# Kernel tuning notes

Hardware: AMD Instinct MI355X
Metric: run time of the kernel (lower is better)

The kernel has to match this reference:

```python
import jax, jax.numpy as jnp
import numpy as np

EMB = 2048
H = 16
Q_RANK = 1536
KV_RANK = 512
ROPE_D = 64
NOPE_D = 64
V_D = 128
QK_D = ROPE_D + NOPE_D  # 128
ROPE_BASE = 10000.0
SCALING = 1.0  # query_pre_attn_scalar ** -0.5 with scalar=1.0


def apply_rope(x):
    """torchtune-style interleaved RoPE. x: (B, S, H, D)."""
    S, D = x.shape[1], x.shape[-1]
    theta = 1.0 / (ROPE_BASE ** (jnp.arange(0, D, 2, dtype=jnp.float32) / D))  # (D/2,)
    ang = jnp.arange(S, dtype=jnp.float32)[:, None] * theta[None, :]  # (S, D/2)
    cos = jnp.cos(ang)[None, :, None, :]
    sin = jnp.sin(ang)[None, :, None, :]
    xf = x.astype(jnp.float32).reshape(*x.shape[:-1], D // 2, 2)
    x0, x1 = xf[..., 0], xf[..., 1]
    out = jnp.stack([x0 * cos - x1 * sin, x1 * cos + x0 * sin], axis=-1)
    return out.reshape(x.shape).astype(x.dtype)


def setup_inputs() -> dict:
    key = jax.random.key(0)
    ks = jax.random.split(key, 6)
    s = lambda fan_in: 1.0 / np.sqrt(fan_in)
    return {
        "x": jax.random.normal(ks[0], (2, 2048, EMB), dtype=jnp.float32),
        "q_a_w": jax.random.uniform(ks[1], (Q_RANK, EMB), jnp.float32, -s(EMB), s(EMB)),
        "q_b_w": jax.random.uniform(ks[2], (H * QK_D, Q_RANK), jnp.float32, -s(Q_RANK), s(Q_RANK)),
        "kv_a_w": jax.random.uniform(ks[3], (KV_RANK + ROPE_D, EMB), jnp.float32, -s(EMB), s(EMB)),
        "kv_b_w": jax.random.uniform(ks[4], (H * (NOPE_D + V_D), KV_RANK), jnp.float32, -s(KV_RANK), s(KV_RANK)),
        "o_w": jax.random.uniform(ks[5], (EMB, H * V_D), jnp.float32, -s(H * V_D), s(H * V_D)),
    }


def reference(x, q_a_w, q_b_w, kv_a_w, kv_b_w, o_w):
    B, S, _ = x.shape
    # LoRA-compressed Q projection
    q = (x @ q_a_w.T) @ q_b_w.T  # (B, S, H*QK_D)
    q = q.reshape(B, S, H, QK_D).transpose(0, 2, 1, 3)  # (B, H, S, QK_D)
    q_pass, q_rot = q[..., :NOPE_D], q[..., NOPE_D:]
    # Compressed KV with shared rope key
    ckv = x @ kv_a_w.T  # (B, S, KV_RANK + ROPE_D)
    k_pass_c, k_rot = ckv[..., :KV_RANK], ckv[..., KV_RANK:]
    kvb = (k_pass_c @ kv_b_w.T).reshape(B, S, H, NOPE_D + V_D).transpose(0, 2, 1, 3)
    k_pass, v = kvb[..., :NOPE_D], kvb[..., NOPE_D:]  # (B,H,S,NOPE_D), (B,H,S,V_D)
    # RoPE (applied in (B,S,H,D) layout, as in the original)
    q_rot = apply_rope(q_rot.transpose(0, 2, 1, 3)).transpose(0, 2, 1, 3)
    k_rot = apply_rope(k_rot[:, :, None, :])  # (B, S, 1, ROPE_D), shared across heads
    k_rot = jnp.broadcast_to(k_rot.transpose(0, 2, 1, 3), (B, H, S, ROPE_D))
    query = jnp.concatenate([q_pass, q_rot], axis=-1)  # (B, H, S, QK_D)
    key = jnp.concatenate([k_pass, k_rot], axis=-1)
    # NOTE: original passes attention_mask=None -> no causal mask applied.
    scores = jnp.einsum("bhqd,bhkd->bhqk", query, key) * SCALING
    attn = jax.nn.softmax(scores.astype(jnp.float32), axis=-1).astype(query.dtype)
    out = jnp.einsum("bhqk,bhkd->bhqd", attn, v)  # (B, H, S, V_D)
    out = out.transpose(0, 2, 1, 3).reshape(B, S, H * V_D)
    return out @ o_w.T
```

## Files before the change

kernel.cpp:

```cpp
#include <hip/hip_runtime.h>
#include <stdint.h>

#define EMB 2048
#define NH 16
#define QRANK 1536
#define KVRANK 512
#define ROPED 64
#define NOPED 64
#define VD 128
#define QKD 128
#define SEQ 2048
#define BATCH 2
#define BS 4096
#define BHD 32
#define NCOMB 2112

typedef __attribute__((ext_vector_type(4))) float f32x4;
typedef __attribute__((ext_vector_type(8))) short s16x8;

__device__ __forceinline__ float bf2f(unsigned short u) {
  return __uint_as_float(((unsigned int)u) << 16);
}
__device__ __forceinline__ unsigned short f2bf(float f) {
  unsigned int u = __float_as_uint(f);
  u += 0x7fff + ((u >> 16) & 1);
  return (unsigned short)(u >> 16);
}

__device__ __forceinline__ void gld_lds16(const unsigned short* g, unsigned short* l) {
  __builtin_amdgcn_global_load_lds((const __attribute__((address_space(1))) void*)g,
                                   (__attribute__((address_space(3))) void*)l,
                                   16, 0, 0);
}

#define N4_X   (BS * EMB / 4)
#define N4_QA  (QRANK * EMB / 4)
#define N4_KVA ((KVRANK + ROPED) * EMB / 4)
#define N4_QB  (NH * QKD * QRANK / 4)
#define N4_KVB (NH * 192 * KVRANK / 4)
#define N4_O   (EMB * NH * VD / 4)
#define N4_TOT (N4_X + N4_QA + N4_KVA + N4_QB + N4_KVB + N4_O)

__global__ void cast_all(const float* __restrict__ x, const float* __restrict__ qa,
                         const float* __restrict__ kva, const float* __restrict__ qb,
                         const float* __restrict__ kvb, const float* __restrict__ ow,
                         unsigned short* __restrict__ Xb, unsigned short* __restrict__ Wcomb,
                         unsigned short* __restrict__ Wqb, unsigned short* __restrict__ Wkvb,
                         unsigned short* __restrict__ Wo) {
  int i = blockIdx.x * blockDim.x + threadIdx.x;
  int stride = gridDim.x * blockDim.x;
  for (; i < N4_TOT; i += stride) {
    const float4* src;
    ushort4* dst;
    int j = i;
    if (j < N4_X) { src = (const float4*)x; dst = (ushort4*)Xb; }
    else if ((j -= N4_X) < N4_QA) { src = (const float4*)qa; dst = (ushort4*)Wcomb; }
    else if ((j -= N4_QA) < N4_KVA) { src = (const float4*)kva; dst = (ushort4*)(Wcomb + (size_t)QRANK * EMB); }
    else if ((j -= N4_KVA) < N4_QB) { src = (const float4*)qb; dst = (ushort4*)Wqb; }
    else if ((j -= N4_QB) < N4_KVB) { src = (const float4*)kvb; dst = (ushort4*)Wkvb; }
    else { j -= N4_KVB; src = (const float4*)ow; dst = (ushort4*)Wo; }
    float4 v = src[j];
    ushort4 o;
    o.x = f2bf(v.x); o.y = f2bf(v.y); o.z = f2bf(v.z); o.w = f2bf(v.w);
    dst[j] = o;
  }
}

template <int OUT_F32>
__global__ __launch_bounds__(256, 2) void gemm_bt(
    const unsigned short* __restrict__ A, int lda,
    const unsigned short* __restrict__ W, int ldw,
    void* __restrict__ C, int M, int N, int K)
{
  __shared__ __align__(16) unsigned short As[128 * 64];
  __shared__ __align__(16) unsigned short Ws[128 * 64];
  const int tid = threadIdx.x;
  const int wave = tid >> 6;
  const int lane = tid & 63;
  const int ln = lane & 15;
  const int quad = lane >> 4;
  const int bm = blockIdx.y * 128;
  const int bn = blockIdx.x * 128;
  const int wm = (wave >> 1) * 64;
  const int wn = (wave & 1) * 64;

  f32x4 acc[4][4] = {};

  const int rel8 = lane >> 3;
  const int csw = ((lane & 7) ^ rel8) * 8;

  for (int k0 = 0; k0 < K; k0 += 64) {
#pragma unroll
    for (int it = 0; it < 4; ++it) {
      int rb = wave * 32 + it * 8;
      gld_lds16(A + (size_t)(bm + rb + rel8) * lda + k0 + csw, &As[rb * 64]);
    }
#pragma unroll
    for (int it = 0; it < 4; ++it) {
      int rb = wave * 32 + it * 8;
      int wr = bn + rb + rel8;
      if (wr >= N) wr = N - 1;
      gld_lds16(W + (size_t)wr * ldw + k0 + csw, &Ws[rb * 64]);
    }
    __syncthreads();
#pragma unroll
    for (int kk = 0; kk < 64; kk += 32) {
      s16x8 a[4], b[4];
#pragma unroll
      for (int mt = 0; mt < 4; ++mt)
        a[mt] = *(const s16x8*)&As[(wm + mt * 16 + ln) * 64 + ((kk / 8 + quad) ^ (ln & 7)) * 8];
#pragma unroll
      for (int nt = 0; nt < 4; ++nt)
        b[nt] = *(const s16x8*)&Ws[(wn + nt * 16 + ln) * 64 + ((kk / 8 + quad) ^ (ln & 7)) * 8];
#pragma unroll
      for (int mt = 0; mt < 4; ++mt)
#pragma unroll
        for (int nt = 0; nt < 4; ++nt)
          acc[mt][nt] = __builtin_amdgcn_mfma_f32_16x16x32_bf16(a[mt], b[nt], acc[mt][nt], 0, 0, 0);
    }
    __syncthreads();
  }
#pragma unroll
  for (int mt = 0; mt < 4; ++mt) {
    int row = bm + wm + mt * 16 + quad * 4;
#pragma unroll
    for (int nt = 0; nt < 4; ++nt) {
      int col = bn + wn + nt * 16 + ln;
      if (col < N) {
#pragma unroll
        for (int r = 0; r < 4; ++r) {
          float v = acc[mt][nt][r];
          if (OUT_F32)
            ((float*)C)[(size_t)(row + r) * N + col] = v;
          else
            ((unsigned short*)C)[(size_t)(row + r) * N + col] = f2bf(v);
        }
      }
    }
  }
}

__global__ __launch_bounds__(256, 2) void gemm_q_rope(
    const unsigned short* __restrict__ A, int lda,
    const unsigned short* __restrict__ W, int ldw,
    unsigned short* __restrict__ Qry, int K)
{
  __shared__ __align__(16) unsigned short As[128 * 64];
  __shared__ __align__(16) unsigned short Ws[128 * 64];
  const int tid = threadIdx.x;
  const int wave = tid >> 6;
  const int lane = tid & 63;
  const int ln = lane & 15;
  const int quad = lane >> 4;
  const int bm = blockIdx.y * 128;
  const int bn = blockIdx.x * 128;
  const int wm = (wave >> 1) * 64;
  const int wn = (wave & 1) * 64;

  f32x4 acc[4][4] = {};
  const int rel8 = lane >> 3;
  const int csw = ((lane & 7) ^ rel8) * 8;

  for (int k0 = 0; k0 < K; k0 += 64) {
#pragma unroll
    for (int it = 0; it < 4; ++it) {
      int rb = wave * 32 + it * 8;
      gld_lds16(A + (size_t)(bm + rb + rel8) * lda + k0 + csw, &As[rb * 64]);
    }
#pragma unroll
    for (int it = 0; it < 4; ++it) {
      int rb = wave * 32 + it * 8;
      gld_lds16(W + (size_t)(bn + rb + rel8) * ldw + k0 + csw, &Ws[rb * 64]);
    }
    __syncthreads();
#pragma unroll
    for (int kk = 0; kk < 64; kk += 32) {
      s16x8 a[4], b[4];
#pragma unroll
      for (int mt = 0; mt < 4; ++mt)
        a[mt] = *(const s16x8*)&As[(wm + mt * 16 + ln) * 64 + ((kk / 8 + quad) ^ (ln & 7)) * 8];
#pragma unroll
      for (int nt = 0; nt < 4; ++nt)
        b[nt] = *(const s16x8*)&Ws[(wn + nt * 16 + ln) * 64 + ((kk / 8 + quad) ^ (ln & 7)) * 8];
#pragma unroll
      for (int mt = 0; mt < 4; ++mt)
#pragma unroll
        for (int nt = 0; nt < 4; ++nt)
          acc[mt][nt] = __builtin_amdgcn_mfma_f32_16x16x32_bf16(a[mt], b[nt], acc[mt][nt], 0, 0, 0);
    }
    __syncthreads();
  }
  const bool odd = (ln & 1);
#pragma unroll
  for (int mt = 0; mt < 4; ++mt) {
    int rowb = bm + wm + mt * 16 + quad * 4;
#pragma unroll
    for (int nt = 0; nt < 4; ++nt) {
      int col = bn + wn + nt * 16 + ln;
      int h = col >> 7, d = col & 127;
#pragma unroll
      for (int r = 0; r < 4; ++r) {
        float v = acc[mt][nt][r];
        float other = __shfl_xor(v, 1);
        int row = rowb + r;
        int b = row >> 11, s = row & 2047;
        float y = v;
        if (d >= NOPED) {
          int i = (d - NOPED) >> 1;
          float theta = exp2f(-(float)i * (13.287712379549449f / 32.f));
          float ang = (float)s * theta;
          float sn, c;
          sincosf(ang, &sn, &c);
          y = v * c + (odd ? other * sn : -other * sn);
        }
        Qry[((size_t)(b * NH + h) * SEQ + s) * QKD + d] = f2bf(y);
      }
    }
  }
}

__global__ void prep_key(const unsigned short* __restrict__ kvb,
                         const unsigned short* __restrict__ cqkv,
                         unsigned short* __restrict__ Key) {
  __shared__ unsigned short krot[ROPED];
  int bs = blockIdx.x;
  int b = bs >> 11, s = bs & 2047;
  int tid = threadIdx.x;
  if (tid < 32) {
    int i = tid;
    float x0 = bf2f(cqkv[(size_t)bs * NCOMB + QRANK + KVRANK + 2 * i]);
    float x1 = bf2f(cqkv[(size_t)bs * NCOMB + QRANK + KVRANK + 2 * i + 1]);
    float theta = exp2f(-(float)i * (13.287712379549449f / 32.f));
    float ang = (float)s * theta;
    float sn, c;
    sincosf(ang, &sn, &c);
    krot[2 * i] = f2bf(x0 * c - x1 * sn);
    krot[2 * i + 1] = f2bf(x1 * c + x0 * sn);
  }
  __syncthreads();
  for (int idx = tid; idx < NH * QKD; idx += 256) {
    int h = idx >> 7, d = idx & 127;
    unsigned short v;
    if (d < NOPED)
      v = kvb[(size_t)bs * (NH * 192) + h * 192 + d];
    else
      v = krot[d - NOPED];
    Key[((size_t)(b * NH + h) * SEQ + s) * QKD + d] = v;
  }
}

__global__ void transpose_v(const unsigned short* __restrict__ kvb, unsigned short* __restrict__ VT) {
  __shared__ unsigned short tile[64][132];
  int blk = blockIdx.x;
  int bh = blk >> 5, st = blk & 31;
  int b = bh >> 4, h = bh & 15;
  int s0 = st * 64;
  int tid = threadIdx.x;
  for (int idx = tid; idx < 64 * 128; idx += 256) {
    int sl = idx >> 7, d = idx & 127;
    tile[sl][d] = kvb[((size_t)(b * SEQ + s0 + sl)) * (NH * 192) + h * 192 + NOPED + d];
  }
  __syncthreads();
  for (int idx = tid; idx < 64 * 128; idx += 256) {
    int d = idx >> 6, sl = idx & 63;
    VT[((size_t)bh * VD + d) * SEQ + s0 + sl] = tile[sl][d];
  }
}

__global__ __launch_bounds__(256, 2) void flash_attn(
    const unsigned short* __restrict__ Q,
    const unsigned short* __restrict__ Kt,
    const unsigned short* __restrict__ VT,
    unsigned short* __restrict__ O)
{
  __shared__ __align__(16) unsigned short Ks[64 * 128];
  __shared__ __align__(16) unsigned short Vs[128 * 64];
  __shared__ __align__(16) unsigned short Ps[4 * 2048];

  const int tid = threadIdx.x;
  const int wave = tid >> 6;
  const int lane = tid & 63;
  const int ln = lane & 15;
  const int quad = lane >> 4;
  const int bh = blockIdx.x;
  const int q0 = blockIdx.y * 128;

  s16x8 qa[2][4];
#pragma unroll
  for (int mt = 0; mt < 2; ++mt) {
    const unsigned short* qrow = Q + ((size_t)bh * SEQ + q0 + wave * 32 + mt * 16 + ln) * QKD;
#pragma unroll
    for (int kx = 0; kx < 4; ++kx)
      qa[mt][kx] = *(const s16x8*)(qrow + kx * 32 + quad * 8);
  }

  unsigned short* Pw = &Ps[wave * 2048];

  f32x4 o[2][8] = {};
  float m_i[2][4], l_i[2][4];
#pragma unroll
  for (int mt = 0; mt < 2; ++mt)
#pragma unroll
    for (int r = 0; r < 4; ++r) { m_i[mt][r] = -1e30f; l_i[mt][r] = 0.f; }

  const bool even = ((ln & 1) == 0);

  for (int kt = 0; kt < SEQ / 64; ++kt) {
    {
      int rel = lane >> 4, cch = lane & 15;
#pragma unroll
      for (int it = 0; it < 4; ++it) {
        int rb = wave * 16 + it * 4;
        int rr = rb + rel;
        int c = cch ^ (rr & 15);
        gld_lds16(Kt + ((size_t)bh * SEQ + kt * 64 + rr) * QKD + c * 8, &Ks[rb * 128]);
      }
      int rel8 = lane >> 3;
      int c8 = (lane & 7) ^ rel8;
#pragma unroll
      for (int it = 0; it < 4; ++it) {
        int rb = wave * 32 + it * 8;
        gld_lds16(VT + ((size_t)bh * VD + rb + rel8) * SEQ + kt * 64 + c8 * 8, &Vs[rb * 64]);
      }
    }
    __syncthreads();

    f32x4 sc[2][4] = {};
#pragma unroll
    for (int kx = 0; kx < 4; ++kx) {
      s16x8 bk[4];
#pragma unroll
      for (int t = 0; t < 4; ++t)
        bk[t] = *(const s16x8*)&Ks[(t * 16 + ln) * 128 + ((kx * 4 + quad) ^ ln) * 8];
#pragma unroll
      for (int mt = 0; mt < 2; ++mt)
#pragma unroll
        for (int t = 0; t < 4; ++t)
          sc[mt][t] = __builtin_amdgcn_mfma_f32_16x16x32_bf16(qa[mt][kx], bk[t], sc[mt][t], 0, 0, 0);
    }

    float al[2][4];
#pragma unroll
    for (int mt = 0; mt < 2; ++mt) {
      float mx[4], rs[4];
#pragma unroll
      for (int r = 0; r < 4; ++r)
        mx[r] = fmaxf(fmaxf(sc[mt][0][r], sc[mt][1][r]), fmaxf(sc[mt][2][r], sc[mt][3][r]));
#pragma unroll
      for (int msk = 1; msk < 16; msk <<= 1)
#pragma unroll
        for (int r = 0; r < 4; ++r)
          mx[r] = fmaxf(mx[r], __shfl_xor(mx[r], msk));
#pragma unroll
      for (int r = 0; r < 4; ++r) {
        float mn = fmaxf(m_i[mt][r], mx[r]);
        al[mt][r] = __expf(m_i[mt][r] - mn);
        m_i[mt][r] = mn;
        rs[r] = 0.f;
      }
#pragma unroll
      for (int t = 0; t < 4; ++t)
#pragma unroll
        for (int r = 0; r < 4; ++r) {
          float e = __expf(sc[mt][t][r] - m_i[mt][r]);
          sc[mt][t][r] = e;
          rs[r] += e;
        }
#pragma unroll
      for (int msk = 1; msk < 16; msk <<= 1)
#pragma unroll
        for (int r = 0; r < 4; ++r)
          rs[r] += __shfl_xor(rs[r], msk);
#pragma unroll
      for (int r = 0; r < 4; ++r)
        l_i[mt][r] = l_i[mt][r] * al[mt][r] + rs[r];
#pragma unroll
      for (int dt = 0; dt < 8; ++dt)
#pragma unroll
        for (int r = 0; r < 4; ++r)
          o[mt][dt][r] *= al[mt][r];
    }

#pragma unroll
    for (int mt = 0; mt < 2; ++mt)
#pragma unroll
      for (int t = 0; t < 4; ++t) {
        unsigned int pu[4], nu[4];
#pragma unroll
        for (int r = 0; r < 4; ++r) {
          pu[r] = __float_as_uint(sc[mt][t][r]);
          nu[r] = __float_as_uint(__shfl_xor(sc[mt][t][r], 1));
        }
        if (even) {
          int cb = t * 2 + (ln >> 3);
          int rbase = mt * 16 + quad * 4;
#pragma unroll
          for (int rp = 0; rp < 2; ++rp) {
            int swc = cb ^ (quad * 2 + rp);
            unsigned short* a = &Pw[(rbase + 2 * rp) * 64 + swc * 8 + (ln & 7)];
            *(unsigned int*)a        = (pu[2 * rp] >> 16)     | (nu[2 * rp] & 0xffff0000u);
            *(unsigned int*)(a + 64) = (pu[2 * rp + 1] >> 16) | (nu[2 * rp + 1] & 0xffff0000u);
          }
        }
      }
    asm volatile("s_waitcnt lgkmcnt(0)" ::: "memory");

#pragma unroll
    for (int kc = 0; kc < 2; ++kc) {
      s16x8 ap[2];
#pragma unroll
      for (int mt = 0; mt < 2; ++mt)
        ap[mt] = *(const s16x8*)&Pw[(mt * 16 + ln) * 64 + ((kc * 4 + quad) ^ (ln >> 1)) * 8];
#pragma unroll
      for (int dt = 0; dt < 8; ++dt) {
        s16x8 bv = *(const s16x8*)&Vs[(dt * 16 + ln) * 64 + ((kc * 4 + quad) ^ (ln & 7)) * 8];
#pragma unroll
        for (int mt = 0; mt < 2; ++mt)
          o[mt][dt] = __builtin_amdgcn_mfma_f32_16x16x32_bf16(ap[mt], bv, o[mt][dt], 0, 0, 0);
      }
    }
    __syncthreads();
  }

  const int b = bh >> 4, h = bh & 15;
#pragma unroll
  for (int mt = 0; mt < 2; ++mt)
#pragma unroll
    for (int r = 0; r < 4; ++r) {
      float inv = 1.f / l_i[mt][r];
      int s = q0 + wave * 32 + mt * 16 + quad * 4 + r;
      size_t rowbase = ((size_t)b * SEQ + s) * (NH * VD) + h * VD;
#pragma unroll
      for (int dt = 0; dt < 8; ++dt)
        O[rowbase + dt * 16 + ln] = f2bf(o[mt][dt][r] * inv);
    }
}

extern "C" void kernel_launch(void* const* d_in, const int* in_sizes, int n_in,
                              void* d_out, int out_size, void* d_ws, size_t ws_size,
                              hipStream_t stream) {
  const float* x_f    = (const float*)d_in[0];
  const float* qaw_f  = (const float*)d_in[1];
  const float* qbw_f  = (const float*)d_in[2];
  const float* kvaw_f = (const float*)d_in[3];
  const float* kvbw_f = (const float*)d_in[4];
  const float* ow_f   = (const float*)d_in[5];

  char* ws = (char*)d_ws;
  size_t off = 0;
  auto alloc = [&](size_t n) {
    unsigned short* p = (unsigned short*)(ws + off);
    off = (off + n * 2 + 255) & ~(size_t)255;
    return p;
  };
  unsigned short* Xb    = alloc((size_t)BS * EMB);
  unsigned short* Wcomb = alloc((size_t)NCOMB * EMB);
  unsigned short* Wqb   = alloc((size_t)(NH * QKD) * QRANK);
  unsigned short* Wkvb  = alloc((size_t)(NH * 192) * KVRANK);
  unsigned short* Wo    = alloc((size_t)EMB * (NH * VD));
  unsigned short* CQKV  = alloc((size_t)BS * NCOMB);
  unsigned short* KVB   = alloc((size_t)BS * (NH * 192));
  unsigned short* Qry   = alloc((size_t)BHD * SEQ * QKD);
  unsigned short* Key   = alloc((size_t)BHD * SEQ * QKD);
  unsigned short* Vt    = alloc((size_t)BHD * VD * SEQ);
  unsigned short* AO    = alloc((size_t)BS * (NH * VD));

  cast_all<<<dim3(8192), 256, 0, stream>>>(x_f, qaw_f, kvaw_f, qbw_f, kvbw_f, ow_f,
                                           Xb, Wcomb, Wqb, Wkvb, Wo);

  gemm_bt<0><<<dim3((NCOMB + 127) / 128, BS / 128), 256, 0, stream>>>(
      Xb, EMB, Wcomb, EMB, CQKV, BS, NCOMB, EMB);
  gemm_q_rope<<<dim3((NH * QKD) / 128, BS / 128), 256, 0, stream>>>(
      CQKV, NCOMB, Wqb, QRANK, Qry, QRANK);
  gemm_bt<0><<<dim3((NH * 192) / 128, BS / 128), 256, 0, stream>>>(
      CQKV + QRANK, NCOMB, Wkvb, KVRANK, KVB, BS, NH * 192, KVRANK);

  prep_key<<<dim3(BS), 256, 0, stream>>>(KVB, CQKV, Key);
  transpose_v<<<dim3(BHD * (SEQ / 64)), 256, 0, stream>>>(KVB, Vt);

  flash_attn<<<dim3(BHD, SEQ / 128), 256, 0, stream>>>(Qry, Key, Vt, AO);

  gemm_bt<1><<<dim3(EMB / 128, BS / 128), 256, 0, stream>>>(
      AO, NH * VD, Wo, NH * VD, d_out, BS, EMB, NH * VD);
}
```

Baseline: 432.7 us.

## Compute transposed scores to keep P in registers, dropping LDS round-trip

```diff
diff --git a/kernel.cpp b/kernel.cpp
--- a/kernel.cpp
+++ b/kernel.cpp
@@ -17,6 +17,7 @@
 
 typedef __attribute__((ext_vector_type(4))) float f32x4;
 typedef __attribute__((ext_vector_type(8))) short s16x8;
+typedef __attribute__((ext_vector_type(4))) short s16x4;
 
 __device__ __forceinline__ float bf2f(unsigned short u) {
   return __uint_as_float(((unsigned int)u) << 16);
@@ -25,6 +26,14 @@
   unsigned int u = __float_as_uint(f);
   u += 0x7fff + ((u >> 16) & 1);
   return (unsigned short)(u >> 16);
+}
+
+__device__ __forceinline__ f32x4 mfma16k16(s16x4 a, s16x4 b, f32x4 c) {
+#if __has_builtin(__builtin_amdgcn_mfma_f32_16x16x16_bf16)
+  return __builtin_amdgcn_mfma_f32_16x16x16_bf16(a, b, c, 0, 0, 0);
+#else
+  return __builtin_amdgcn_mfma_f32_16x16x16bf16_1k(a, b, c, 0, 0, 0);
+#endif
 }
 
 __device__ __forceinline__ void gld_lds16(const unsigned short* g, unsigned short* l) {
@@ -275,7 +284,6 @@
 {
   __shared__ __align__(16) unsigned short Ks[64 * 128];
   __shared__ __align__(16) unsigned short Vs[128 * 64];
-  __shared__ __align__(16) unsigned short Ps[4 * 2048];
 
   const int tid = threadIdx.x;
   const int wave = tid >> 6;
@@ -294,16 +302,9 @@
       qa[mt][kx] = *(const s16x8*)(qrow + kx * 32 + quad * 8);
   }
 
-  unsigned short* Pw = &Ps[wave * 2048];
-
   f32x4 o[2][8] = {};
-  float m_i[2][4], l_i[2][4];
-#pragma unroll
-  for (int mt = 0; mt < 2; ++mt)
-#pragma unroll
-    for (int r = 0; r < 4; ++r) { m_i[mt][r] = -1e30f; l_i[mt][r] = 0.f; }
-
-  const bool even = ((ln & 1) == 0);
+  float m_i[2] = {-1e30f, -1e30f};
+  float l_i[2] = {0.f, 0.f};
 
   for (int kt = 0; kt < SEQ / 64; ++kt) {
     {
@@ -328,95 +329,63 @@
     f32x4 sc[2][4] = {};
 #pragma unroll
     for (int kx = 0; kx < 4; ++kx) {
-      s16x8 bk[4];
+      s16x8 ak[4];
 #pragma unroll
       for (int t = 0; t < 4; ++t)
-        bk[t] = *(const s16x8*)&Ks[(t * 16 + ln) * 128 + ((kx * 4 + quad) ^ ln) * 8];
+        ak[t] = *(const s16x8*)&Ks[(t * 16 + ln) * 128 + ((kx * 4 + quad) ^ ln) * 8];
 #pragma unroll
       for (int mt = 0; mt < 2; ++mt)
 #pragma unroll
         for (int t = 0; t < 4; ++t)
-          sc[mt][t] = __builtin_amdgcn_mfma_f32_16x16x32_bf16(qa[mt][kx], bk[t], sc[mt][t], 0, 0, 0);
-    }
-
-    float al[2][4];
+          sc[mt][t] = __builtin_amdgcn_mfma_f32_16x16x32_bf16(ak[t], qa[mt][kx], sc[mt][t], 0, 0, 0);
+    }
+
+    s16x4 pb[2][4];
 #pragma unroll
     for (int mt = 0; mt < 2; ++mt) {
-      float mx[4], rs[4];
-#pragma unroll
-      for (int r = 0; r < 4; ++r)
-        mx[r] = fmaxf(fmaxf(sc[mt][0][r], sc[mt][1][r]), fmaxf(sc[mt][2][r], sc[mt][3][r]));
-#pragma unroll
-      for (int msk = 1; msk < 16; msk <<= 1)
+      float mx = sc[mt][0][0];
+#pragma unroll
+      for (int t = 0; t < 4; ++t)
 #pragma unroll
         for (int r = 0; r < 4; ++r)
-          mx[r] = fmaxf(mx[r], __shfl_xor(mx[r], msk));
-#pragma unroll
-      for (int r = 0; r < 4; ++r) {
-        float mn = fmaxf(m_i[mt][r], mx[r]);
-        al[mt][r] = __expf(m_i[mt][r] - mn);
-        m_i[mt][r] = mn;
-        rs[r] = 0.f;
-      }
-#pragma unroll
-      for (int t = 0; t < 4; ++t)
-#pragma unroll
-        for (int r = 0; r < 4; ++r) {
-          float e = __expf(sc[mt][t][r] - m_i[mt][r]);
-          sc[mt][t][r] = e;
-          rs[r] += e;
-        }
-#pragma unroll
-      for (int msk = 1; msk < 16; msk <<= 1)
+          mx = fmaxf(mx, sc[mt][t][r]);
+      mx = fmaxf(mx, __shfl_xor(mx, 16));
+      mx = fmaxf(mx, __shfl_xor(mx, 32));
+      float mn = fmaxf(m_i[mt], mx);
+      float al = __expf(m_i[mt] - mn);
+      m_i[mt] = mn;
+      float rs = 0.f;
+#pragma unroll
+      for (int t = 0; t < 4; ++t) {
+        float e0 = __expf(sc[mt][t][0] - mn);
+        float e1 = __expf(sc[mt][t][1] - mn);
+        float e2 = __expf(sc[mt][t][2] - mn);
+        float e3 = __expf(sc[mt][t][3] - mn);
+        rs += (e0 + e1) + (e2 + e3);
+        s16x4 p;
+        p[0] = (short)f2bf(e0); p[1] = (short)f2bf(e1);
+        p[2] = (short)f2bf(e2); p[3] = (short)f2bf(e3);
+        pb[mt][t] = p;
+      }
+      rs += __shfl_xor(rs, 16);
+      rs += __shfl_xor(rs, 32);
+      l_i[mt] = l_i[mt] * al + rs;
+#pragma unroll
+      for (int dt = 0; dt < 8; ++dt)
 #pragma unroll
         for (int r = 0; r < 4; ++r)
-          rs[r] += __shfl_xor(rs[r], msk);
-#pragma unroll
-      for (int r = 0; r < 4; ++r)
-        l_i[mt][r] = l_i[mt][r] * al[mt][r] + rs[r];
-#pragma unroll
-      for (int dt = 0; dt < 8; ++dt)
-#pragma unroll
-        for (int r = 0; r < 4; ++r)
-          o[mt][dt][r] *= al[mt][r];
-    }
-
-#pragma unroll
-    for (int mt = 0; mt < 2; ++mt)
-#pragma unroll
-      for (int t = 0; t < 4; ++t) {
-        unsigned int pu[4], nu[4];
-#pragma unroll
-        for (int r = 0; r < 4; ++r) {
-          pu[r] = __float_as_uint(sc[mt][t][r]);
-          nu[r] = __float_as_uint(__shfl_xor(sc[mt][t][r], 1));
-        }
-        if (even) {
-          int cb = t * 2 + (ln >> 3);
-          int rbase = mt * 16 + quad * 4;
-#pragma unroll
-          for (int rp = 0; rp < 2; ++rp) {
-            int swc = cb ^ (quad * 2 + rp);
-            unsigned short* a = &Pw[(rbase + 2 * rp) * 64 + swc * 8 + (ln & 7)];
-            *(unsigned int*)a        = (pu[2 * rp] >> 16)     | (nu[2 * rp] & 0xffff0000u);
-            *(unsigned int*)(a + 64) = (pu[2 * rp + 1] >> 16) | (nu[2 * rp + 1] & 0xffff0000u);
-          }
-        }
-      }
-    asm volatile("s_waitcnt lgkmcnt(0)" ::: "memory");
-
-#pragma unroll
-    for (int kc = 0; kc < 2; ++kc) {
-      s16x8 ap[2];
-#pragma unroll
-      for (int mt = 0; mt < 2; ++mt)
-        ap[mt] = *(const s16x8*)&Pw[(mt * 16 + ln) * 64 + ((kc * 4 + quad) ^ (ln >> 1)) * 8];
+          o[mt][dt][r] *= al;
+    }
+
+#pragma unroll
+    for (int kc = 0; kc < 4; ++kc) {
+      int gsl = ((kc * 2 + (quad >> 1)) ^ (ln & 7)) * 8 + (quad & 1) * 4;
 #pragma unroll
       for (int dt = 0; dt < 8; ++dt) {
-        s16x8 bv = *(const s16x8*)&Vs[(dt * 16 + ln) * 64 + ((kc * 4 + quad) ^ (ln & 7)) * 8];
+        s16x4 av = *(const s16x4*)&Vs[(dt * 16 + ln) * 64 + gsl];
 #pragma unroll
         for (int mt = 0; mt < 2; ++mt)
-          o[mt][dt] = __builtin_amdgcn_mfma_f32_16x16x32_bf16(ap[mt], bv, o[mt][dt], 0, 0, 0);
+          o[mt][dt] = mfma16k16(av, pb[mt][kc], o[mt][dt]);
       }
     }
     __syncthreads();
@@ -424,16 +393,20 @@
 
   const int b = bh >> 4, h = bh & 15;
 #pragma unroll
-  for (int mt = 0; mt < 2; ++mt)
-#pragma unroll
-    for (int r = 0; r < 4; ++r) {
-      float inv = 1.f / l_i[mt][r];
-      int s = q0 + wave * 32 + mt * 16 + quad * 4 + r;
-      size_t rowbase = ((size_t)b * SEQ + s) * (NH * VD) + h * VD;
-#pragma unroll
-      for (int dt = 0; dt < 8; ++dt)
-        O[rowbase + dt * 16 + ln] = f2bf(o[mt][dt][r] * inv);
-    }
+  for (int mt = 0; mt < 2; ++mt) {
+    float inv = 1.f / l_i[mt];
+    int s = q0 + wave * 32 + mt * 16 + ln;
+    size_t rowbase = ((size_t)b * SEQ + s) * (NH * VD) + h * VD;
+#pragma unroll
+    for (int dt = 0; dt < 8; ++dt) {
+      ushort4 pk;
+      pk.x = f2bf(o[mt][dt][0] * inv);
+      pk.y = f2bf(o[mt][dt][1] * inv);
+      pk.z = f2bf(o[mt][dt][2] * inv);
+      pk.w = f2bf(o[mt][dt][3] * inv);
+      *(ushort4*)&O[rowbase + dt * 16 + quad * 4] = pk;
+    }
+  }
 }
 
 extern "C" void kernel_launch(void* const* d_in, const int* in_sizes, int n_in,
```

New measurement: 399.6 us. 7.7% less time.
